# Performance work log

Measured on AMD Instinct MI355X. Metric: run time of the kernel, lower is better.

Reference implementation:

```python
import jax, jax.numpy as jnp
import numpy as np

HIDDEN = 2048
INTER = 768
N_EXPERTS = 64
TOP_K = 8
BATCH, SEQ = 2, 2048


def setup_inputs() -> dict:
    key = jax.random.key(0)
    k_x, k_g, k_gp, k_up, k_dp = jax.random.split(key, 5)
    s_in = 1.0 / np.sqrt(HIDDEN)   # lecun_normal fan_in scaling
    s_mid = 1.0 / np.sqrt(INTER)
    return {
        "x": jax.random.normal(k_x, (BATCH, SEQ, HIDDEN), dtype=jnp.float32),
        "gate_w": jax.random.normal(k_g, (HIDDEN, N_EXPERTS), dtype=jnp.float32) * s_in,
        "gate_proj": jax.random.normal(k_gp, (N_EXPERTS, HIDDEN, INTER), dtype=jnp.float32) * s_in,
        "up_proj": jax.random.normal(k_up, (N_EXPERTS, HIDDEN, INTER), dtype=jnp.float32) * s_in,
        "down_proj": jax.random.normal(k_dp, (N_EXPERTS, INTER, HIDDEN), dtype=jnp.float32) * s_mid,
    }


def reference(x, gate_w, gate_proj, up_proj, down_proj):
    H = x.shape[-1]
    E = gate_proj.shape[0]
    K = TOP_K

    x_flat = x.reshape(-1, H)                      # [T, H]
    router_logits = x_flat @ gate_w                # [T, E]

    routing_weights, selected_experts = jax.lax.top_k(router_logits, k=K)  # [T, K]
    routing_weights = jax.nn.softmax(routing_weights, axis=-1)

    sel_flat = jnp.ravel(selected_experts)         # [T*K]
    x_expanded = jnp.repeat(x_flat, K, axis=0)     # [T*K, H]

    sort_idx = jnp.argsort(sel_flat)
    unsort_idx = jnp.argsort(sort_idx)
    x_sorted = x_expanded[sort_idx]                # tokens grouped by expert
    group_sizes = jnp.bincount(sel_flat, length=E)

    gate_out = jax.lax.ragged_dot(x_sorted, gate_proj, group_sizes)  # [T*K, I]
    up_out = jax.lax.ragged_dot(x_sorted, up_proj, group_sizes)      # [T*K, I]
    activated = jax.nn.silu(gate_out) * up_out
    down_out = jax.lax.ragged_dot(activated, down_proj, group_sizes)  # [T*K, H]

    unsorted = down_out[unsort_idx].reshape(-1, K, H)  # [T, K, H]
    out = (unsorted * routing_weights[..., None]).sum(axis=1)
    return out.reshape(x.shape), router_logits
```

## Files before the change

kernel.cpp:

```cpp
#include <hip/hip_runtime.h>
#include <hip/hip_bf16.h>
#include <cstdint>

#define NTOK 4096
#define HID  2048
#define ITER 768
#define NEXP 64
#define TOPK 8
#define MAXT 320

typedef __attribute__((ext_vector_type(8))) short sh8;
typedef __attribute__((ext_vector_type(4))) float f32x4;

#define MFMA16 __builtin_amdgcn_mfma_f32_16x16x32_bf16

__device__ __forceinline__ uint16_t f2b(float f) {
  union { float f; uint32_t u; } v; v.f = f;
  uint32_t u = v.u;
  u += 0x7FFFu + ((u >> 16) & 1u);
  return (uint16_t)(u >> 16);
}

__device__ __forceinline__ float b2f_lo(uint32_t w) {
  union { uint32_t u; float f; } v; v.u = w << 16; return v.f;
}
__device__ __forceinline__ float b2f_hi(uint32_t w) {
  union { uint32_t u; float f; } v; v.u = w & 0xffff0000u; return v.f;
}

__device__ __forceinline__ uint32_t cvtpk(float lo, float hi) {
  float2 f2; f2.x = lo; f2.y = hi;
  __hip_bfloat162 h = __float22bfloat162_rn(f2);
  union { __hip_bfloat162 h; uint32_t u; } v; v.h = h;
  return v.u;
}

__device__ __forceinline__ void gl2lds16(const void* g, void* l) {
  __builtin_amdgcn_global_load_lds(
      (const __attribute__((address_space(1))) uint32_t*)g,
      (__attribute__((address_space(3))) uint32_t*)l, 16, 0, 0);
}

__device__ __forceinline__ int xcd_unswizzle(int s, int na) {
  int q = na >> 3, r = na & 7, x = s & 7, i = s >> 3;
  return (x < r ? x * (q + 1) : r * (q + 1) + (x - r) * q) + i;
}

__global__ void zero_kernel(int* __restrict__ cc) {
  cc[threadIdx.x] = 0;
}

__global__ __launch_bounds__(256) void xcast_kernel(const float* __restrict__ x,
                                                    uint16_t* __restrict__ xb) {
  size_t i = ((size_t)blockIdx.x * 256 + threadIdx.x) * 8;
  float4 a = *(const float4*)(x + i);
  float4 b = *(const float4*)(x + i + 4);
  uint4 o;
  o.x = (uint32_t)f2b(a.x) | ((uint32_t)f2b(a.y) << 16);
  o.y = (uint32_t)f2b(a.z) | ((uint32_t)f2b(a.w) << 16);
  o.z = (uint32_t)f2b(b.x) | ((uint32_t)f2b(b.y) << 16);
  o.w = (uint32_t)f2b(b.z) | ((uint32_t)f2b(b.w) << 16);
  *(uint4*)(xb + i) = o;
}

__global__ __launch_bounds__(256) void router_kernel(
    const float* __restrict__ x, const float* __restrict__ gate_w,
    float* __restrict__ logits, int* __restrict__ topk_id,
    float* __restrict__ topk_w, int* __restrict__ counts)
{
  int lane = threadIdx.x & 63;
  int wv   = threadIdx.x >> 6;
  int t    = blockIdx.x * 4 + wv;
  const float* xr = x + (size_t)t * HID;
  float acc = 0.f;
  #pragma unroll 4
  for (int h = 0; h < HID; h += 4) {
    float4 xv = *(const float4*)(xr + h);
    acc += xv.x * gate_w[(h + 0) * NEXP + lane];
    acc += xv.y * gate_w[(h + 1) * NEXP + lane];
    acc += xv.z * gate_w[(h + 2) * NEXP + lane];
    acc += xv.w * gate_w[(h + 3) * NEXP + lane];
  }
  logits[(size_t)t * NEXP + lane] = acc;

  float v = acc;
  float topv[TOPK]; int topi[TOPK];
  #pragma unroll
  for (int k = 0; k < TOPK; ++k) {
    float bv = v; int bi = lane;
    #pragma unroll
    for (int off = 32; off > 0; off >>= 1) {
      float ov = __shfl_xor(bv, off);
      int   oi = __shfl_xor(bi, off);
      if (ov > bv || (ov == bv && oi < bi)) { bv = ov; bi = oi; }
    }
    topv[k] = bv; topi[k] = bi;
    if (lane == bi) v = -3.0e38f;
  }
  float m = topv[0], s = 0.f, w[TOPK];
  #pragma unroll
  for (int k = 0; k < TOPK; ++k) { w[k] = __expf(topv[k] - m); s += w[k]; }
  float inv = 1.f / s;
  if (lane < TOPK) {
    topk_id[t * TOPK + lane] = topi[lane];
    topk_w[t * TOPK + lane]  = w[lane] * inv;
    atomicAdd(&counts[topi[lane]], 1);
  }
}

__global__ void offsets_kernel(const int* __restrict__ counts, int* __restrict__ offsets,
                               int* __restrict__ tiles, int* __restrict__ tilecount) {
  if (threadIdx.x == 0) {
    int s = 0, nt = 0;
    for (int e = 0; e < NEXP; ++e) {
      offsets[e] = s;
      int c = counts[e];
      for (int rb = 0; rb * 256 < c; ++rb) tiles[nt++] = (e << 16) | rb;
      s += c;
    }
    offsets[NEXP] = s;
    tilecount[0] = nt;
  }
}

__global__ __launch_bounds__(256) void scatter_kernel(
    const int* __restrict__ topk_id,
    const int* __restrict__ offsets, int* __restrict__ cursor,
    int* __restrict__ pair_tok, int* __restrict__ inv)
{
  int p = blockIdx.x * 256 + threadIdx.x;
  int e = topk_id[p];
  int pos = offsets[e] + atomicAdd(&cursor[e], 1);
  pair_tok[pos] = p;
  inv[p] = pos;
}

__global__ __launch_bounds__(1024, 4) void gateup_kernel(
    const uint16_t* __restrict__ xb,
    const float* __restrict__ gate_proj,
    const float* __restrict__ up_proj,
    const int* __restrict__ pair_tok,
    const int* __restrict__ offsets,
    const int* __restrict__ tiles,
    const int* __restrict__ tilecount,
    uint16_t* __restrict__ act)
{
  const int nt = tilecount[0];
  const int na = nt * 6;
  if (blockIdx.x >= na) return;
  const int L  = xcd_unswizzle(blockIdx.x, na);
  const int ti = L % nt, nc = L / nt;
  const int te = tiles[ti];
  const int e = te >> 16, row0 = (te & 0xffff) * 256;
  const int start = offsets[e];
  const int count = offsets[e + 1] - start;
  const int nvalid = min(256, count - row0);

  __shared__ __align__(16) uint16_t aT[256 * 64];
  __shared__ __align__(16) uint16_t bT[256 * 64];
  __shared__ int s_tok[256];

  const int t = threadIdx.x, l = t & 63, w = t >> 6;
  if (t < 256)
    s_tok[t] = (t < nvalid) ? (pair_tok[start + row0 + t] >> 3) : 0;
  __syncthreads();

  const int sub = l >> 3;
  const int xk  = ((l & 7) ^ sub) << 3;
  const uint16_t* srcA[2]; char* dstA[2];
  #pragma unroll
  for (int q = 0; q < 2; ++q) {
    int rl = (w * 2 + q) * 8 + sub;
    srcA[q] = xb + (size_t)s_tok[rl] * HID + xk;
    dstA[q] = (char*)aT + (w * 2 + q) * 1024;
  }

  const int brow = t & 255;
  const int kk0  = (t >> 8) * 16;
  const int rcomb  = nc * 256 + brow;
  const int n_orig = ((rcomb >> 5) << 4) + (rcomb & 15);
  const int is_up  = (rcomb >> 4) & 1;
  const float* wsrc = (is_up ? up_proj : gate_proj)
                    + (size_t)e * HID * ITER + n_orig;
  uint16_t* bwr[2];
  #pragma unroll
  for (int s = 0; s < 2; ++s) {
    int kb = (kk0 * 2 + 16 * s) ^ ((brow & 7) << 4);
    bwr[s] = (uint16_t*)((char*)bT + brow * 128 + kb);
  }

  const int wr = w >> 2, wc = w & 3, lr = l & 15, hi = l >> 4;
  const int xorv = (lr & 7) << 4;

  f32x4 acc[4][4];
  #pragma unroll
  for (int mi = 0; mi < 4; ++mi)
    #pragma unroll
    for (int ni = 0; ni < 4; ++ni)
      acc[mi][ni] = (f32x4){0.f, 0.f, 0.f, 0.f};

  float va[16];
  {
    const float* wp = wsrc + (size_t)kk0 * ITER;
    #pragma unroll
    for (int j = 0; j < 16; ++j) va[j] = wp[(size_t)j * ITER];
  }

  for (int kc = 0; kc < 32; ++kc) {
    __syncthreads();
    {
      uint4 o0, o1;
      o0.x = cvtpk(va[0],  va[1]);  o0.y = cvtpk(va[2],  va[3]);
      o0.z = cvtpk(va[4],  va[5]);  o0.w = cvtpk(va[6],  va[7]);
      o1.x = cvtpk(va[8],  va[9]);  o1.y = cvtpk(va[10], va[11]);
      o1.z = cvtpk(va[12], va[13]); o1.w = cvtpk(va[14], va[15]);
      *(uint4*)bwr[0] = o0;
      *(uint4*)bwr[1] = o1;
    }
    #pragma unroll
    for (int q = 0; q < 2; ++q)
      gl2lds16(srcA[q] + kc * 64, dstA[q]);
    __syncthreads();
    if (kc + 1 < 32) {
      const float* wp = wsrc + (size_t)((kc + 1) * 64 + kk0) * ITER;
      #pragma unroll
      for (int j = 0; j < 16; ++j) va[j] = wp[(size_t)j * ITER];
    }
    __builtin_amdgcn_sched_barrier(0);
    #pragma unroll
    for (int ks = 0; ks < 2; ++ks) {
      sh8 af[4], bf[4];
      #pragma unroll
      for (int mi = 0; mi < 4; ++mi)
        af[mi] = *(const sh8*)((const char*)aT +
                   (wr * 64 + mi * 16 + lr) * 128 + ((ks * 64 + hi * 16) ^ xorv));
      #pragma unroll
      for (int ni = 0; ni < 4; ++ni)
        bf[ni] = *(const sh8*)((const char*)bT +
                   (wc * 64 + ni * 16 + lr) * 128 + ((ks * 64 + hi * 16) ^ xorv));
      #pragma unroll
      for (int mi = 0; mi < 4; ++mi)
        #pragma unroll
        for (int ni = 0; ni < 4; ++ni)
          acc[mi][ni] = MFMA16(af[mi], bf[ni], acc[mi][ni], 0, 0, 0);
    }
  }

  #pragma unroll
  for (int mi = 0; mi < 4; ++mi)
    #pragma unroll
    for (int p = 0; p < 2; ++p)
      #pragma unroll
      for (int j = 0; j < 4; ++j) {
        int row = wr * 64 + mi * 16 + hi * 4 + j;
        if (row < nvalid) {
          float g = acc[mi][2 * p][j], u = acc[mi][2 * p + 1][j];
          float a = (g / (1.f + __expf(-g))) * u;
          int col = nc * 128 + (wc * 2 + p) * 16 + lr;
          act[(size_t)(start + row0 + row) * ITER + col] = f2b(a);
        }
      }
}

__global__ __launch_bounds__(1024, 4) void down_kernel(
    const uint16_t* __restrict__ act,
    const float* __restrict__ down_proj,
    const int* __restrict__ offsets,
    const int* __restrict__ tiles,
    const int* __restrict__ tilecount,
    uint16_t* __restrict__ dd)
{
  const int nt = tilecount[0];
  const int na = nt * 8;
  if (blockIdx.x >= na) return;
  const int L  = xcd_unswizzle(blockIdx.x, na);
  const int ti = L % nt, nc = L / nt;
  const int te = tiles[ti];
  const int e = te >> 16, row0 = (te & 0xffff) * 256;
  const int start = offsets[e];
  const int count = offsets[e + 1] - start;
  const int nvalid = min(256, count - row0);

  __shared__ __align__(16) uint16_t aT[256 * 64];
  __shared__ __align__(16) uint16_t bT[256 * 64];

  const int t = threadIdx.x, l = t & 63, w = t >> 6;

  const int sub = l >> 3;
  const int xk  = ((l & 7) ^ sub) << 3;

  const uint16_t* srcA[2]; char* dstA[2];
  #pragma unroll
  for (int q = 0; q < 2; ++q) {
    int rl = (w * 2 + q) * 8 + sub;
    srcA[q] = act + (size_t)(start + row0 + rl) * ITER + xk;
    dstA[q] = (char*)aT + (w * 2 + q) * 1024;
  }

  const int brow = t & 255;
  const int kk0  = (t >> 8) * 16;
  const float* wsrc = down_proj + (size_t)e * ITER * HID + nc * 256 + brow;
  uint16_t* bwr[2];
  #pragma unroll
  for (int s = 0; s < 2; ++s) {
    int kb = (kk0 * 2 + 16 * s) ^ ((brow & 7) << 4);
    bwr[s] = (uint16_t*)((char*)bT + brow * 128 + kb);
  }

  const int wr = w >> 2, wc = w & 3, lr = l & 15, hi = l >> 4;
  const int xorv = (lr & 7) << 4;

  f32x4 acc[4][4];
  #pragma unroll
  for (int mi = 0; mi < 4; ++mi)
    #pragma unroll
    for (int ni = 0; ni < 4; ++ni)
      acc[mi][ni] = (f32x4){0.f, 0.f, 0.f, 0.f};

  float va[16];
  {
    const float* wp = wsrc + (size_t)kk0 * HID;
    #pragma unroll
    for (int j = 0; j < 16; ++j) va[j] = wp[(size_t)j * HID];
  }

  for (int kc = 0; kc < 12; ++kc) {
    __syncthreads();
    {
      uint4 o0, o1;
      o0.x = cvtpk(va[0],  va[1]);  o0.y = cvtpk(va[2],  va[3]);
      o0.z = cvtpk(va[4],  va[5]);  o0.w = cvtpk(va[6],  va[7]);
      o1.x = cvtpk(va[8],  va[9]);  o1.y = cvtpk(va[10], va[11]);
      o1.z = cvtpk(va[12], va[13]); o1.w = cvtpk(va[14], va[15]);
      *(uint4*)bwr[0] = o0;
      *(uint4*)bwr[1] = o1;
    }
    #pragma unroll
    for (int q = 0; q < 2; ++q)
      gl2lds16(srcA[q] + kc * 64, dstA[q]);
    __syncthreads();
    if (kc + 1 < 12) {
      const float* wp = wsrc + (size_t)((kc + 1) * 64 + kk0) * HID;
      #pragma unroll
      for (int j = 0; j < 16; ++j) va[j] = wp[(size_t)j * HID];
    }
    __builtin_amdgcn_sched_barrier(0);
    #pragma unroll
    for (int ks = 0; ks < 2; ++ks) {
      sh8 af[4], bf[4];
      #pragma unroll
      for (int mi = 0; mi < 4; ++mi)
        af[mi] = *(const sh8*)((const char*)aT +
                   (wr * 64 + mi * 16 + lr) * 128 + ((ks * 64 + hi * 16) ^ xorv));
      #pragma unroll
      for (int ni = 0; ni < 4; ++ni)
        bf[ni] = *(const sh8*)((const char*)bT +
                   (wc * 64 + ni * 16 + lr) * 128 + ((ks * 64 + hi * 16) ^ xorv));
      #pragma unroll
      for (int mi = 0; mi < 4; ++mi)
        #pragma unroll
        for (int ni = 0; ni < 4; ++ni)
          acc[mi][ni] = MFMA16(af[mi], bf[ni], acc[mi][ni], 0, 0, 0);
    }
  }

  #pragma unroll
  for (int mi = 0; mi < 4; ++mi)
    #pragma unroll
    for (int ni = 0; ni < 4; ++ni)
      #pragma unroll
      for (int j = 0; j < 4; ++j) {
        int row = wr * 64 + mi * 16 + hi * 4 + j;
        if (row < nvalid) {
          int col = nc * 256 + wc * 64 + ni * 16 + lr;
          dd[(size_t)(start + row0 + row) * HID + col] = f2b(acc[mi][ni][j]);
        }
      }
}

__global__ __launch_bounds__(256) void reduce_kernel(
    const uint16_t* __restrict__ dd, const float* __restrict__ topk_w,
    const int* __restrict__ inv, float* __restrict__ out)
{
  const int tok = blockIdx.x;
  const int c   = threadIdx.x * 8;
  float acc[8] = {0.f, 0.f, 0.f, 0.f, 0.f, 0.f, 0.f, 0.f};
  #pragma unroll
  for (int k = 0; k < TOPK; ++k) {
    const int   pos = inv[tok * TOPK + k];
    const float wk  = topk_w[tok * TOPK + k];
    uint4 v = *(const uint4*)&dd[(size_t)pos * HID + c];
    acc[0] += wk * b2f_lo(v.x);  acc[1] += wk * b2f_hi(v.x);
    acc[2] += wk * b2f_lo(v.y);  acc[3] += wk * b2f_hi(v.y);
    acc[4] += wk * b2f_lo(v.z);  acc[5] += wk * b2f_hi(v.z);
    acc[6] += wk * b2f_lo(v.w);  acc[7] += wk * b2f_hi(v.w);
  }
  float4 o0 = {acc[0], acc[1], acc[2], acc[3]};
  float4 o1 = {acc[4], acc[5], acc[6], acc[7]};
  float* op = out + (size_t)tok * HID + c;
  *(float4*)op       = o0;
  *(float4*)(op + 4) = o1;
}

extern "C" void kernel_launch(void* const* d_in, const int* in_sizes, int n_in,
                              void* d_out, int out_size, void* d_ws, size_t ws_size,
                              hipStream_t stream) {
  const float* x         = (const float*)d_in[0];
  const float* gate_w    = (const float*)d_in[1];
  const float* gate_proj = (const float*)d_in[2];
  const float* up_proj   = (const float*)d_in[3];
  const float* down_proj = (const float*)d_in[4];

  float* out    = (float*)d_out;
  float* logits = out + (size_t)NTOK * HID;

  char* ws = (char*)d_ws;
  size_t off = 0;
  uint16_t* xb      = (uint16_t*)(ws + off); off += (size_t)NTOK * HID * 2;
  uint16_t* act     = (uint16_t*)(ws + off); off += (size_t)(NTOK * TOPK + 256) * ITER * 2;
  uint16_t* dd      = (uint16_t*)(ws + off); off += (size_t)(NTOK * TOPK + 256) * HID * 2;
  int*      topk_id = (int*)  (ws + off); off += (size_t)NTOK * TOPK * 4;
  float*    topk_w  = (float*)(ws + off); off += (size_t)NTOK * TOPK * 4;
  int*      counts  = (int*)  (ws + off); off += 256;
  int*      cursor  = (int*)  (ws + off); off += 256;
  int*      offsets = (int*)  (ws + off); off += 512;
  int*      tiles   = (int*)  (ws + off); off += MAXT * 4;
  int*      tilecount=(int*)  (ws + off); off += 256;
  int*      pair_tok= (int*)  (ws + off); off += (size_t)NTOK * TOPK * 4;
  int*      inv     = (int*)  (ws + off); off += (size_t)NTOK * TOPK * 4;

  zero_kernel   <<<1,    128, 0, stream>>>(counts);
  xcast_kernel  <<<4096, 256, 0, stream>>>(x, xb);
  router_kernel <<<1024, 256, 0, stream>>>(x, gate_w, logits, topk_id, topk_w, counts);
  offsets_kernel<<<1,    64,  0, stream>>>(counts, offsets, tiles, tilecount);
  scatter_kernel<<<128,  256, 0, stream>>>(topk_id, offsets, cursor, pair_tok, inv);

  gateup_kernel<<<MAXT * 6, 1024, 0, stream>>>(xb, gate_proj, up_proj, pair_tok, offsets,
                                               tiles, tilecount, act);
  down_kernel  <<<MAXT * 8, 1024, 0, stream>>>(act, down_proj, offsets,
                                               tiles, tilecount, dd);
  reduce_kernel<<<NTOK, 256, 0, stream>>>(dd, topk_w, inv, out);
}
```

Measured before the change: 803.1 us.

## Double-buffer LDS tiles in expert GEMMs with one barrier per k-step

Both grouped GEMM kernels now use two LDS buffers for the A and B tiles. Each iteration writes the next tile while MFMAs consume the current one, and the two __syncthreads per iteration become one barrier preceded by a partial vmcnt wait. This keeps the global weight prefetch in flight across the compute. The prefetch distance grows to two steps, and MFMA sections get raised wave priority. LDS use doubles to about 128KB per block, which may cut occupancy, and the hand-written waitcnt relies on an exact count of outstanding loads.

Result: slower. 872.7 us (+8.7%).

```diff
diff --git a/kernel.cpp b/kernel.cpp
--- a/kernel.cpp
+++ b/kernel.cpp
@@ -156,8 +156,8 @@
   const int count = offsets[e + 1] - start;
   const int nvalid = min(256, count - row0);
 
-  __shared__ __align__(16) uint16_t aT[256 * 64];
-  __shared__ __align__(16) uint16_t bT[256 * 64];
+  __shared__ __align__(16) uint16_t aT[2 * 256 * 64];
+  __shared__ __align__(16) uint16_t bT[2 * 256 * 64];
   __shared__ int s_tok[256];
 
   const int t = threadIdx.x, l = t & 63, w = t >> 6;
@@ -201,42 +201,63 @@
 
   float va[16];
   {
-    const float* wp = wsrc + (size_t)kk0 * ITER;
-    #pragma unroll
-    for (int j = 0; j < 16; ++j) va[j] = wp[(size_t)j * ITER];
-  }
+    float v0[16];
+    const float* wp0 = wsrc + (size_t)kk0 * ITER;
+    #pragma unroll
+    for (int j = 0; j < 16; ++j) v0[j] = wp0[(size_t)j * ITER];
+    {
+      uint4 o0, o1;
+      o0.x = cvtpk(v0[0],  v0[1]);  o0.y = cvtpk(v0[2],  v0[3]);
+      o0.z = cvtpk(v0[4],  v0[5]);  o0.w = cvtpk(v0[6],  v0[7]);
+      o1.x = cvtpk(v0[8],  v0[9]);  o1.y = cvtpk(v0[10], v0[11]);
+      o1.z = cvtpk(v0[12], v0[13]); o1.w = cvtpk(v0[14], v0[15]);
+      *(uint4*)bwr[0] = o0;
+      *(uint4*)bwr[1] = o1;
+    }
+    #pragma unroll
+    for (int q = 0; q < 2; ++q) gl2lds16(srcA[q], dstA[q]);
+    const float* wp1 = wsrc + (size_t)(64 + kk0) * ITER;
+    #pragma unroll
+    for (int j = 0; j < 16; ++j) va[j] = wp1[(size_t)j * ITER];
+  }
+  __builtin_amdgcn_sched_barrier(0);
+  asm volatile("s_waitcnt vmcnt(16) lgkmcnt(0)");
+  __builtin_amdgcn_s_barrier();
 
   for (int kc = 0; kc < 32; ++kc) {
-    __syncthreads();
+    const int cur = kc & 1, nxt = cur ^ 1;
+    const int k1 = min(kc + 1, 31), k2 = min(kc + 2, 31);
     {
       uint4 o0, o1;
       o0.x = cvtpk(va[0],  va[1]);  o0.y = cvtpk(va[2],  va[3]);
       o0.z = cvtpk(va[4],  va[5]);  o0.w = cvtpk(va[6],  va[7]);
       o1.x = cvtpk(va[8],  va[9]);  o1.y = cvtpk(va[10], va[11]);
       o1.z = cvtpk(va[12], va[13]); o1.w = cvtpk(va[14], va[15]);
-      *(uint4*)bwr[0] = o0;
-      *(uint4*)bwr[1] = o1;
+      *(uint4*)(bwr[0] + nxt * 16384) = o0;
+      *(uint4*)(bwr[1] + nxt * 16384) = o1;
     }
     #pragma unroll
     for (int q = 0; q < 2; ++q)
-      gl2lds16(srcA[q] + kc * 64, dstA[q]);
-    __syncthreads();
-    if (kc + 1 < 32) {
-      const float* wp = wsrc + (size_t)((kc + 1) * 64 + kk0) * ITER;
+      gl2lds16(srcA[q] + k1 * 64, dstA[q] + nxt * 32768);
+    {
+      const float* wp = wsrc + (size_t)(k2 * 64 + kk0) * ITER;
       #pragma unroll
       for (int j = 0; j < 16; ++j) va[j] = wp[(size_t)j * ITER];
     }
     __builtin_amdgcn_sched_barrier(0);
+    __builtin_amdgcn_s_setprio(1);
+    const char* aBuf = (const char*)aT + cur * 32768;
+    const char* bBuf = (const char*)bT + cur * 32768;
     #pragma unroll
     for (int ks = 0; ks < 2; ++ks) {
       sh8 af[4], bf[4];
       #pragma unroll
       for (int mi = 0; mi < 4; ++mi)
-        af[mi] = *(const sh8*)((const char*)aT +
+        af[mi] = *(const sh8*)(aBuf +
                    (wr * 64 + mi * 16 + lr) * 128 + ((ks * 64 + hi * 16) ^ xorv));
       #pragma unroll
       for (int ni = 0; ni < 4; ++ni)
-        bf[ni] = *(const sh8*)((const char*)bT +
+        bf[ni] = *(const sh8*)(bBuf +
                    (wc * 64 + ni * 16 + lr) * 128 + ((ks * 64 + hi * 16) ^ xorv));
       #pragma unroll
       for (int mi = 0; mi < 4; ++mi)
@@ -244,6 +265,10 @@
         for (int ni = 0; ni < 4; ++ni)
           acc[mi][ni] = MFMA16(af[mi], bf[ni], acc[mi][ni], 0, 0, 0);
     }
+    __builtin_amdgcn_s_setprio(0);
+    __builtin_amdgcn_sched_barrier(0);
+    asm volatile("s_waitcnt vmcnt(16) lgkmcnt(0)");
+    __builtin_amdgcn_s_barrier();
   }
 
   #pragma unroll
@@ -281,8 +306,8 @@
   const int count = offsets[e + 1] - start;
   const int nvalid = min(256, count - row0);
 
-  __shared__ __align__(16) uint16_t aT[256 * 64];
-  __shared__ __align__(16) uint16_t bT[256 * 64];
+  __shared__ __align__(16) uint16_t aT[2 * 256 * 64];
+  __shared__ __align__(16) uint16_t bT[2 * 256 * 64];
 
   const int t = threadIdx.x, l = t & 63, w = t >> 6;
 
@@ -319,42 +344,63 @@
 
   float va[16];
   {
-    const float* wp = wsrc + (size_t)kk0 * HID;
-    #pragma unroll
-    for (int j = 0; j < 16; ++j) va[j] = wp[(size_t)j * HID];
-  }
+    float v0[16];
+    const float* wp0 = wsrc + (size_t)kk0 * HID;
+    #pragma unroll
+    for (int j = 0; j < 16; ++j) v0[j] = wp0[(size_t)j * HID];
+    {
+      uint4 o0, o1;
+      o0.x = cvtpk(v0[0],  v0[1]);  o0.y = cvtpk(v0[2],  v0[3]);
+      o0.z = cvtpk(v0[4],  v0[5]);  o0.w = cvtpk(v0[6],  v0[7]);
+      o1.x = cvtpk(v0[8],  v0[9]);  o1.y = cvtpk(v0[10], v0[11]);
+      o1.z = cvtpk(v0[12], v0[13]); o1.w = cvtpk(v0[14], v0[15]);
+      *(uint4*)bwr[0] = o0;
+      *(uint4*)bwr[1] = o1;
+    }
+    #pragma unroll
+    for (int q = 0; q < 2; ++q) gl2lds16(srcA[q], dstA[q]);
+    const float* wp1 = wsrc + (size_t)(64 + kk0) * HID;
+    #pragma unroll
+    for (int j = 0; j < 16; ++j) va[j] = wp1[(size_t)j * HID];
+  }
+  __builtin_amdgcn_sched_barrier(0);
+  asm volatile("s_waitcnt vmcnt(16) lgkmcnt(0)");
+  __builtin_amdgcn_s_barrier();
 
   for (int kc = 0; kc < 12; ++kc) {
-    __syncthreads();
+    const int cur = kc & 1, nxt = cur ^ 1;
+    const int k1 = min(kc + 1, 11), k2 = min(kc + 2, 11);
     {
       uint4 o0, o1;
       o0.x = cvtpk(va[0],  va[1]);  o0.y = cvtpk(va[2],  va[3]);
       o0.z = cvtpk(va[4],  va[5]);  o0.w = cvtpk(va[6],  va[7]);
       o1.x = cvtpk(va[8],  va[9]);  o1.y = cvtpk(va[10], va[11]);
       o1.z = cvtpk(va[12], va[13]); o1.w = cvtpk(va[14], va[15]);
-      *(uint4*)bwr[0] = o0;
-      *(uint4*)bwr[1] = o1;
+      *(uint4*)(bwr[0] + nxt * 16384) = o0;
+      *(uint4*)(bwr[1] + nxt * 16384) = o1;
     }
     #pragma unroll
     for (int q = 0; q < 2; ++q)
-      gl2lds16(srcA[q] + kc * 64, dstA[q]);
-    __syncthreads();
-    if (kc + 1 < 12) {
-      const float* wp = wsrc + (size_t)((kc + 1) * 64 + kk0) * HID;
+      gl2lds16(srcA[q] + k1 * 64, dstA[q] + nxt * 32768);
+    {
+      const float* wp = wsrc + (size_t)(k2 * 64 + kk0) * HID;
       #pragma unroll
       for (int j = 0; j < 16; ++j) va[j] = wp[(size_t)j * HID];
     }
     __builtin_amdgcn_sched_barrier(0);
+    __builtin_amdgcn_s_setprio(1);
+    const char* aBuf = (const char*)aT + cur * 32768;
+    const char* bBuf = (const char*)bT + cur * 32768;
     #pragma unroll
     for (int ks = 0; ks < 2; ++ks) {
       sh8 af[4], bf[4];
       #pragma unroll
       for (int mi = 0; mi < 4; ++mi)
-        af[mi] = *(const sh8*)((const char*)aT +
+        af[mi] = *(const sh8*)(aBuf +
                    (wr * 64 + mi * 16 + lr) * 128 + ((ks * 64 + hi * 16) ^ xorv));
       #pragma unroll
       for (int ni = 0; ni < 4; ++ni)
-        bf[ni] = *(const sh8*)((const char*)bT +
+        bf[ni] = *(const sh8*)(bBuf +
                    (wc * 64 + ni * 16 + lr) * 128 + ((ks * 64 + hi * 16) ^ xorv));
       #pragma unroll
       for (int mi = 0; mi < 4; ++mi)
@@ -362,6 +408,10 @@
         for (int ni = 0; ni < 4; ++ni)
           acc[mi][ni] = MFMA16(af[mi], bf[ni], acc[mi][ni], 0, 0, 0);
     }
+    __builtin_amdgcn_s_setprio(0);
+    __builtin_amdgcn_sched_barrier(0);
+    asm volatile("s_waitcnt vmcnt(16) lgkmcnt(0)");
+    __builtin_amdgcn_s_barrier();
   }
 
   #pragma unroll
```
